# Performance work log

Measured on AMD Instinct MI355X. Metric: run time of the kernel, lower is better.

## Reference

```python
import jax, jax.numpy as jnp
import numpy as np

B, L, E, H, D = 32, 512, 256, 8, 64
SCALE = int(D ** 0.5)  # matches TF: int(hidden_dim ** 0.5) == 8


def setup_inputs() -> dict:
    key = jax.random.key(0)
    ks = jax.random.split(key, 6)
    return {
        "x": jax.random.normal(ks[0], (B, L, E), dtype=jnp.float32),
        "positional": jax.random.normal(ks[1], (L, E), dtype=jnp.float32) * 0.02,
        "Wq": jax.random.normal(ks[2], (H, E, D), dtype=jnp.float32) * 0.05,
        "Wk": jax.random.normal(ks[3], (H, E, D), dtype=jnp.float32) * 0.05,
        "Wv": jax.random.normal(ks[4], (H, E, D), dtype=jnp.float32) * 0.05,
        "Wo": jax.random.normal(ks[5], (H * D, E), dtype=jnp.float32) * 0.05,
    }


def reference(x, positional, Wq, Wk, Wv, Wo):
    act = jnp.tanh  # activation='tanh'
    xp = x + positional                                   # [B,L,E]
    # Batched per-head projections with activation applied post-matmul
    q = act(jnp.einsum('ble,hed->bhld', xp, Wq))          # [B,H,L,D]
    k = act(jnp.einsum('ble,hed->bhld', xp, Wk))
    v = act(jnp.einsum('ble,hed->bhld', xp, Wv))
    score = jnp.einsum('bhqd,bhkd->bhqk', q, k) / SCALE   # [B,H,L,L]
    attn = jax.nn.softmax(score, axis=-1)
    out = jnp.einsum('bhqk,bhkd->bhqd', attn, v)          # [B,H,L,D]
    # concat heads along last axis (head-major) -> [B,L,H*D]
    out = jnp.transpose(out, (0, 2, 1, 3)).reshape(B, L, H * D)
    return jnp.einsum('blf,fe->ble', out, Wo) + act(xp)   # [B,L,E]
```

## Files before the change

kernel.cpp:

```cpp
#include <hip/hip_runtime.h>
#include <cstdint>

#define NB 32
#define NL 512
#define NE 256
#define NH 8
#define ND 64
#define NM 16384
#define NHD 512

using half8  = __attribute__((ext_vector_type(8))) _Float16;
using half4  = __attribute__((ext_vector_type(4))) _Float16;
using f32x4  = __attribute__((ext_vector_type(4))) float;
using f32x16 = __attribute__((ext_vector_type(16))) float;

__device__ __forceinline__ f32x4 mfma16(half8 a, half8 b, f32x4 c) {
    return __builtin_amdgcn_mfma_f32_16x16x32_f16(a, b, c, 0, 0, 0);
}
__device__ __forceinline__ f32x16 mfma32(half8 a, half8 b, f32x16 c) {
    return __builtin_amdgcn_mfma_f32_32x32x16_f16(a, b, c, 0, 0, 0);
}
__device__ __forceinline__ void cp16_g2l(const void* g, void* l) {
    __builtin_amdgcn_global_load_lds(
        (const __attribute__((address_space(1))) void*)g,
        (__attribute__((address_space(3))) void*)l, 16, 0, 0);
}
__device__ __forceinline__ float fast_tanh(float x) {
    float xc = fminf(fmaxf(x, -9.f), 9.f);
    float t = __expf(2.f * xc);
    return (t - 1.f) * __builtin_amdgcn_rcpf(t + 1.f);
}

__global__ __launch_bounds__(256) void prep(
        const float* __restrict__ x, const float* __restrict__ pos,
        const float* __restrict__ Wq, const float* __restrict__ Wk,
        const float* __restrict__ Wv, const float* __restrict__ Wo,
        _Float16* __restrict__ wqkv, _Float16* __restrict__ woh,
        _Float16* __restrict__ xph) {
    int bid = blockIdx.x;
    if (bid < 2048) {
        int idx = bid * 256 + threadIdx.x;
        if (idx < 1536 * 256) {
            int n = idx >> 8, e = idx & 255;
            int s = n >> 9, h = (n >> 6) & 7, d = n & 63;
            const float* W = (s == 0) ? Wq : (s == 1) ? Wk : Wv;
            wqkv[idx] = (_Float16)W[(h * NE + e) * ND + d];
        } else {
            int j = idx - 1536 * 256;
            int e = j >> 9, f = j & 511;
            woh[j] = (_Float16)Wo[f * NE + e];
        }
    } else {
        int i = ((bid - 2048) * 256 + threadIdx.x) * 4;
        float4 xv = *(const float4*)(x + i);
        float4 pv = *(const float4*)(pos + (i & (NL * NE - 1)));
        half4 o;
        o[0] = (_Float16)(xv.x + pv.x);
        o[1] = (_Float16)(xv.y + pv.y);
        o[2] = (_Float16)(xv.z + pv.z);
        o[3] = (_Float16)(xv.w + pv.w);
        *(half4*)(xph + i) = o;
    }
}

__global__ __launch_bounds__(256) void proj_gemm(
        const _Float16* __restrict__ wqkv, const _Float16* __restrict__ xph,
        _Float16* __restrict__ q_all, _Float16* __restrict__ k_all,
        _Float16* __restrict__ vT) {
    __shared__ _Float16 Alds[128 * 64];
    __shared__ _Float16 Blds[128 * 64];
    int tid = threadIdx.x;
    int w = tid >> 6, l = tid & 63;
    int bid = blockIdx.x;
    int xcd = bid & 7, local = bid >> 3;
    int tn = local % 12;
    int tm = xcd * 16 + local / 12;
    int wn = w >> 1, wm = w & 1;
    int m16 = l & 15, g = l >> 4;
    bool isv = (tn >= 8);
    int lrow8 = l >> 3;
    int kc16 = (l & 7) ^ lrow8;
    f32x4 acc[4][4] = {};

    for (int kt = 0; kt < 4; ++kt) {
#pragma unroll
        for (int i = 0; i < 4; ++i) {
            int cA = w * 4 + i;
            int row = cA * 8 + lrow8;
            cp16_g2l(wqkv + (size_t)(tn * 128 + row) * 256 + kt * 64 + kc16 * 8,
                     Alds + cA * 512);
            cp16_g2l(xph + (size_t)(tm * 128 + row) * 256 + kt * 64 + kc16 * 8,
                     Blds + cA * 512);
        }
        __syncthreads();
#pragma unroll
        for (int ks = 0; ks < 2; ++ks) {
            half8 af[4], bf[4];
#pragma unroll
            for (int f = 0; f < 4; ++f) {
                int ra = wn * 64 + f * 16 + m16;
                int rb = wm * 64 + f * 16 + m16;
                af[f] = *(const half8*)(Alds + ra * 64 + (((ks * 4 + g) ^ (ra & 7)) << 3));
                bf[f] = *(const half8*)(Blds + rb * 64 + (((ks * 4 + g) ^ (rb & 7)) << 3));
            }
            if (!isv) {
#pragma unroll
                for (int nf = 0; nf < 4; ++nf)
#pragma unroll
                    for (int mf = 0; mf < 4; ++mf)
                        acc[nf][mf] = mfma16(af[nf], bf[mf], acc[nf][mf]);
            } else {
#pragma unroll
                for (int nf = 0; nf < 4; ++nf)
#pragma unroll
                    for (int mf = 0; mf < 4; ++mf)
                        acc[nf][mf] = mfma16(bf[mf], af[nf], acc[nf][mf]);
            }
        }
        __syncthreads();
    }
    if (!isv) {
        _Float16* dst = (tn < 4) ? q_all : k_all;
#pragma unroll
        for (int nf = 0; nf < 4; ++nf) {
            int c = (tn & 3) * 128 + wn * 64 + nf * 16 + g * 4;
#pragma unroll
            for (int mf = 0; mf < 4; ++mf) {
                int m = tm * 128 + wm * 64 + mf * 16 + m16;
                f32x4 v = acc[nf][mf];
                half4 hv;
#pragma unroll
                for (int r = 0; r < 4; ++r) hv[r] = (_Float16)fast_tanh(v[r]);
                *(half4*)(dst + (size_t)m * NHD + c) = hv;
            }
        }
    } else {
#pragma unroll
        for (int nf = 0; nf < 4; ++nf) {
            int c = (tn - 8) * 128 + wn * 64 + nf * 16 + m16;
#pragma unroll
            for (int mf = 0; mf < 4; ++mf) {
                int t0 = tm * 128 + wm * 64 + mf * 16 + g * 4;
                f32x4 v = acc[nf][mf];
                half4 hv;
#pragma unroll
                for (int r = 0; r < 4; ++r) hv[r] = (_Float16)fast_tanh(v[r]);
                *(half4*)(vT + (size_t)c * NM + t0) = hv;
            }
        }
    }
}

__global__ __launch_bounds__(256, 3) void attn_kernel(
        const _Float16* __restrict__ q_all, const _Float16* __restrict__ k_all,
        const _Float16* __restrict__ vT, _Float16* __restrict__ attn_out) {
    __shared__ _Float16 Klds[2][64 * 64];
    __shared__ _Float16 Vtlds[2][64 * 64];
    __shared__ _Float16 Plds[4][32 * 64];
    int tid = threadIdx.x;
    int w = tid >> 6, l = tid & 63;
    int l31 = l & 31, hi = l >> 5;
    int bid = blockIdx.x;
    int qt = bid & 3, h = (bid >> 2) & 7, b = bid >> 5;

    int qbase = qt * 128 + w * 32;
    half8 qf[4];
    {
        const _Float16* qp = q_all + (size_t)(b * NL + qbase + l31) * NHD + h * ND + hi * 8;
#pragma unroll
        for (int ks = 0; ks < 4; ++ks) qf[ks] = *(const half8*)(qp + ks * 16);
    }

    f32x16 acc_o[2] = {};
    float mrow = -1e30f, lrow = 0.f;

    int st_row = tid >> 2;
    int st_u0 = (tid & 3) * 2;
    const _Float16* kg = k_all + (size_t)(b * NL + st_row) * NHD + h * ND + st_u0 * 8;
    const _Float16* vg = vT + (size_t)(h * ND + st_row) * NM + b * NL + st_u0 * 8;
    int so0 = st_row * 64 + ((st_u0 ^ (st_row & 7)) << 3);
    int so1 = st_row * 64 + (((st_u0 + 1) ^ (st_row & 7)) << 3);

    uint4 kv0 = *(const uint4*)(kg);
    uint4 kv1 = *(const uint4*)(kg + 8);
    uint4 vv0 = *(const uint4*)(vg);
    uint4 vv1 = *(const uint4*)(vg + 8);
    *(uint4*)&Klds[0][so0] = kv0;   *(uint4*)&Klds[0][so1] = kv1;
    *(uint4*)&Vtlds[0][so0] = vv0;  *(uint4*)&Vtlds[0][so1] = vv1;
    __syncthreads();

    for (int kt = 0; kt < 8; ++kt) {
        int cur = kt & 1;
        if (kt < 7) {
            const _Float16* kp = kg + (size_t)(kt + 1) * 64 * NHD;
            const _Float16* vp = vg + (kt + 1) * 64;
            kv0 = *(const uint4*)(kp);      kv1 = *(const uint4*)(kp + 8);
            vv0 = *(const uint4*)(vp);      vv1 = *(const uint4*)(vp + 8);
        }
        f32x16 acc_s[2] = {};
#pragma unroll
        for (int ks = 0; ks < 4; ++ks)
#pragma unroll
            for (int kb2 = 0; kb2 < 2; ++kb2) {
                int key = kb2 * 32 + l31;
                half8 kb = *(const half8*)(&Klds[cur][key * 64 + (((ks * 2 + hi) ^ (key & 7)) << 3)]);
                acc_s[kb2] = mfma32(kb, qf[ks], acc_s[kb2]);
            }
        float mx = -1e30f;
#pragma unroll
        for (int kb2 = 0; kb2 < 2; ++kb2)
#pragma unroll
            for (int j = 0; j < 16; ++j) mx = fmaxf(mx, acc_s[kb2][j]);
        mx = fmaxf(mx, __shfl_xor(mx, 32));
        mx *= 0.125f;
        if (!__all(mx <= mrow + 8.f)) {
            float mn = fmaxf(mrow, mx);
            float alpha = __expf(mrow - mn);
            mrow = mn;
            lrow *= alpha;
            float aq[16];
#pragma unroll
            for (int c = 0; c < 4; ++c)
#pragma unroll
                for (int r = 0; r < 4; ++r)
                    aq[c * 4 + r] = __shfl(alpha, c * 8 + hi * 4 + r);
#pragma unroll
            for (int d2 = 0; d2 < 2; ++d2)
#pragma unroll
                for (int j = 0; j < 16; ++j) acc_o[d2][j] *= aq[j];
        }
        float rs = 0.f;
#pragma unroll
        for (int kb2 = 0; kb2 < 2; ++kb2)
#pragma unroll
            for (int c = 0; c < 4; ++c) {
                half4 hv;
#pragma unroll
                for (int r = 0; r < 4; ++r) {
                    float p = __expf(acc_s[kb2][c * 4 + r] * 0.125f - mrow);
                    rs += p;
                    hv[r] = (_Float16)p;
                }
                int u = kb2 * 4 + c;
                *(half4*)(&Plds[w][l31 * 64 + ((u ^ (l31 & 7)) << 3) + hi * 4]) = hv;
            }
        rs += __shfl_xor(rs, 32);
        lrow += rs;
#pragma unroll
        for (int ks = 0; ks < 4; ++ks) {
            half8 pa = *(const half8*)(&Plds[w][l31 * 64 + (((ks * 2 + hi) ^ (l31 & 7)) << 3)]);
#pragma unroll
            for (int d2 = 0; d2 < 2; ++d2) {
                int d = d2 * 32 + l31;
                half8 vb = *(const half8*)(&Vtlds[cur][d * 64 + (((ks * 2 + hi) ^ (d & 7)) << 3)]);
                acc_o[d2] = mfma32(pa, vb, acc_o[d2]);
            }
        }
        if (kt < 7) {
            int nxt = cur ^ 1;
            *(uint4*)&Klds[nxt][so0] = kv0;   *(uint4*)&Klds[nxt][so1] = kv1;
            *(uint4*)&Vtlds[nxt][so0] = vv0;  *(uint4*)&Vtlds[nxt][so1] = vv1;
            __syncthreads();
        }
    }
    size_t orow0 = (size_t)(b * NL + qbase);
#pragma unroll
    for (int c = 0; c < 4; ++c)
#pragma unroll
        for (int r = 0; r < 4; ++r) {
            int qrow = c * 8 + hi * 4 + r;
            float inv = 1.f / __shfl(lrow, qrow);
#pragma unroll
            for (int d2 = 0; d2 < 2; ++d2)
                attn_out[(orow0 + qrow) * NHD + h * ND + d2 * 32 + l31] =
                    (_Float16)(acc_o[d2][c * 4 + r] * inv);
        }
}

__global__ __launch_bounds__(256) void final_gemm(
        const _Float16* __restrict__ woh, const _Float16* __restrict__ attn,
        const float* __restrict__ x, const float* __restrict__ pos,
        float* __restrict__ out) {
    __shared__ _Float16 Alds[128 * 64];
    __shared__ _Float16 Blds[64 * 64];
    int tid = threadIdx.x;
    int w = tid >> 6, l = tid & 63;
    int tn = blockIdx.x & 1, tm = blockIdx.x >> 1;
    int wn = w >> 1, wm = w & 1;
    int m16 = l & 15, g = l >> 4;
    int lrow8 = l >> 3;
    int kc16 = (l & 7) ^ lrow8;
    f32x4 acc[4][2] = {};

    for (int kt = 0; kt < 8; ++kt) {
#pragma unroll
        for (int i = 0; i < 4; ++i) {
            int cA = w * 4 + i;
            int row = cA * 8 + lrow8;
            cp16_g2l(woh + (size_t)(tn * 128 + row) * 512 + kt * 64 + kc16 * 8,
                     Alds + cA * 512);
        }
#pragma unroll
        for (int i = 0; i < 2; ++i) {
            int cB = w * 2 + i;
            int row = cB * 8 + lrow8;
            cp16_g2l(attn + (size_t)(tm * 64 + row) * 512 + kt * 64 + kc16 * 8,
                     Blds + cB * 512);
        }
        __syncthreads();
#pragma unroll
        for (int ks = 0; ks < 2; ++ks) {
            half8 af[4], bf[2];
#pragma unroll
            for (int f = 0; f < 4; ++f) {
                int ra = wn * 64 + f * 16 + m16;
                af[f] = *(const half8*)(Alds + ra * 64 + (((ks * 4 + g) ^ (ra & 7)) << 3));
            }
#pragma unroll
            for (int f = 0; f < 2; ++f) {
                int rb = wm * 32 + f * 16 + m16;
                bf[f] = *(const half8*)(Blds + rb * 64 + (((ks * 4 + g) ^ (rb & 7)) << 3));
            }
#pragma unroll
            for (int nf = 0; nf < 4; ++nf)
#pragma unroll
                for (int mf = 0; mf < 2; ++mf)
                    acc[nf][mf] = mfma16(af[nf], bf[mf], acc[nf][mf]);
        }
        __syncthreads();
    }
#pragma unroll
    for (int nf = 0; nf < 4; ++nf) {
        int e = tn * 128 + wn * 64 + nf * 16 + g * 4;
#pragma unroll
        for (int mf = 0; mf < 2; ++mf) {
            int m = tm * 64 + wm * 32 + mf * 16 + m16;
            int lr = m & (NL - 1);
            float4 xv = *(const float4*)(x + (size_t)m * NE + e);
            float4 pv = *(const float4*)(pos + (size_t)lr * NE + e);
            f32x4 v = acc[nf][mf];
            float4 o;
            o.x = v[0] + fast_tanh(xv.x + pv.x);
            o.y = v[1] + fast_tanh(xv.y + pv.y);
            o.z = v[2] + fast_tanh(xv.z + pv.z);
            o.w = v[3] + fast_tanh(xv.w + pv.w);
            *(float4*)(out + (size_t)m * NE + e) = o;
        }
    }
}

extern "C" void kernel_launch(void* const* d_in, const int* in_sizes, int n_in,
                              void* d_out, int out_size, void* d_ws, size_t ws_size,
                              hipStream_t stream) {
    const float* x   = (const float*)d_in[0];
    const float* pos = (const float*)d_in[1];
    const float* Wq  = (const float*)d_in[2];
    const float* Wk  = (const float*)d_in[3];
    const float* Wv  = (const float*)d_in[4];
    const float* Wo  = (const float*)d_in[5];
    float* out = (float*)d_out;

    char* ws = (char*)d_ws;
    _Float16* xph   = (_Float16*)(ws);
    _Float16* wqkv  = (_Float16*)(ws + 8388608);
    _Float16* woh   = (_Float16*)(ws + 9175040);
    _Float16* q_all = (_Float16*)(ws + 9437184);
    _Float16* k_all = (_Float16*)(ws + 26214400);
    _Float16* vT    = (_Float16*)(ws + 42991616);
    _Float16* attn  = (_Float16*)(ws + 59768832);

    prep<<<dim3(6144), dim3(256), 0, stream>>>(x, pos, Wq, Wk, Wv, Wo, wqkv, woh, xph);
    proj_gemm<<<dim3(12 * 128), dim3(256), 0, stream>>>(wqkv, xph, q_all, k_all, vT);
    attn_kernel<<<dim3(1024), dim3(256), 0, stream>>>(q_all, k_all, vT, attn);
    final_gemm<<<dim3(512), dim3(256), 0, stream>>>(woh, attn, x, pos, out);
}
```

Baseline: 84.27 us.

## Double-buffer GEMM LDS tiles, raise MFMA priority, reuse fp16 xp in epilogue

```diff
diff --git a/kernel.cpp b/kernel.cpp
--- a/kernel.cpp
+++ b/kernel.cpp
@@ -67,8 +67,8 @@
         const _Float16* __restrict__ wqkv, const _Float16* __restrict__ xph,
         _Float16* __restrict__ q_all, _Float16* __restrict__ k_all,
         _Float16* __restrict__ vT) {
-    __shared__ _Float16 Alds[128 * 64];
-    __shared__ _Float16 Blds[128 * 64];
+    __shared__ _Float16 Alds[2][128 * 64];
+    __shared__ _Float16 Blds[2][128 * 64];
     int tid = threadIdx.x;
     int w = tid >> 6, l = tid & 63;
     int bid = blockIdx.x;
@@ -82,17 +82,24 @@
     int kc16 = (l & 7) ^ lrow8;
     f32x4 acc[4][4] = {};
 
+    const _Float16* Ag = wqkv + (size_t)tn * 128 * 256;
+    const _Float16* Bg = xph + (size_t)tm * 128 * 256;
+
+#define PROJ_STAGE(kt, buf)                                                   \
+    _Pragma("unroll") for (int i = 0; i < 4; ++i) {                           \
+        int cA = w * 4 + i;                                                   \
+        int row = cA * 8 + lrow8;                                             \
+        cp16_g2l(Ag + (size_t)row * 256 + (kt) * 64 + kc16 * 8,               \
+                 &Alds[buf][cA * 512]);                                       \
+        cp16_g2l(Bg + (size_t)row * 256 + (kt) * 64 + kc16 * 8,               \
+                 &Blds[buf][cA * 512]);                                       \
+    }
+
+    PROJ_STAGE(0, 0);
+    __syncthreads();
+    int cur = 0;
     for (int kt = 0; kt < 4; ++kt) {
-#pragma unroll
-        for (int i = 0; i < 4; ++i) {
-            int cA = w * 4 + i;
-            int row = cA * 8 + lrow8;
-            cp16_g2l(wqkv + (size_t)(tn * 128 + row) * 256 + kt * 64 + kc16 * 8,
-                     Alds + cA * 512);
-            cp16_g2l(xph + (size_t)(tm * 128 + row) * 256 + kt * 64 + kc16 * 8,
-                     Blds + cA * 512);
-        }
-        __syncthreads();
+        if (kt < 3) { PROJ_STAGE(kt + 1, cur ^ 1); }
 #pragma unroll
         for (int ks = 0; ks < 2; ++ks) {
             half8 af[4], bf[4];
@@ -100,8 +107,8 @@
             for (int f = 0; f < 4; ++f) {
                 int ra = wn * 64 + f * 16 + m16;
                 int rb = wm * 64 + f * 16 + m16;
-                af[f] = *(const half8*)(Alds + ra * 64 + (((ks * 4 + g) ^ (ra & 7)) << 3));
-                bf[f] = *(const half8*)(Blds + rb * 64 + (((ks * 4 + g) ^ (rb & 7)) << 3));
+                af[f] = *(const half8*)(&Alds[cur][ra * 64 + (((ks * 4 + g) ^ (ra & 7)) << 3)]);
+                bf[f] = *(const half8*)(&Blds[cur][rb * 64 + (((ks * 4 + g) ^ (rb & 7)) << 3)]);
             }
             if (!isv) {
 #pragma unroll
@@ -118,7 +125,9 @@
             }
         }
         __syncthreads();
-    }
+        cur ^= 1;
+    }
+#undef PROJ_STAGE
     if (!isv) {
         _Float16* dst = (tn < 4) ? q_all : k_all;
 #pragma unroll
@@ -198,6 +207,7 @@
             vv0 = *(const uint4*)(vp);      vv1 = *(const uint4*)(vp + 8);
         }
         f32x16 acc_s[2] = {};
+        __builtin_amdgcn_s_setprio(1);
 #pragma unroll
         for (int ks = 0; ks < 4; ++ks)
 #pragma unroll
@@ -206,6 +216,7 @@
                 half8 kb = *(const half8*)(&Klds[cur][key * 64 + (((ks * 2 + hi) ^ (key & 7)) << 3)]);
                 acc_s[kb2] = mfma32(kb, qf[ks], acc_s[kb2]);
             }
+        __builtin_amdgcn_s_setprio(0);
         float mx = -1e30f;
 #pragma unroll
         for (int kb2 = 0; kb2 < 2; ++kb2)
@@ -246,6 +257,7 @@
             }
         rs += __shfl_xor(rs, 32);
         lrow += rs;
+        __builtin_amdgcn_s_setprio(1);
 #pragma unroll
         for (int ks = 0; ks < 4; ++ks) {
             half8 pa = *(const half8*)(&Plds[w][l31 * 64 + (((ks * 2 + hi) ^ (l31 & 7)) << 3)]);
@@ -256,6 +268,7 @@
                 acc_o[d2] = mfma32(pa, vb, acc_o[d2]);
             }
         }
+        __builtin_amdgcn_s_setprio(0);
         if (kt < 7) {
             int nxt = cur ^ 1;
             *(uint4*)&Klds[nxt][so0] = kv0;   *(uint4*)&Klds[nxt][so1] = kv1;
@@ -279,10 +292,9 @@
 
 __global__ __launch_bounds__(256) void final_gemm(
         const _Float16* __restrict__ woh, const _Float16* __restrict__ attn,
-        const float* __restrict__ x, const float* __restrict__ pos,
-        float* __restrict__ out) {
-    __shared__ _Float16 Alds[128 * 64];
-    __shared__ _Float16 Blds[64 * 64];
+        const _Float16* __restrict__ xph, float* __restrict__ out) {
+    __shared__ _Float16 Alds[2][128 * 64];
+    __shared__ _Float16 Blds[2][64 * 64];
     int tid = threadIdx.x;
     int w = tid >> 6, l = tid & 63;
     int tn = blockIdx.x & 1, tm = blockIdx.x >> 1;
@@ -292,34 +304,40 @@
     int kc16 = (l & 7) ^ lrow8;
     f32x4 acc[4][2] = {};
 
+    const _Float16* Ag = woh + (size_t)tn * 128 * 512;
+    const _Float16* Bg = attn + (size_t)tm * 64 * 512;
+
+#define FIN_STAGE(kt, buf)                                                    \
+    _Pragma("unroll") for (int i = 0; i < 4; ++i) {                           \
+        int cA = w * 4 + i;                                                   \
+        int row = cA * 8 + lrow8;                                             \
+        cp16_g2l(Ag + (size_t)row * 512 + (kt) * 64 + kc16 * 8,               \
+                 &Alds[buf][cA * 512]);                                       \
+    }                                                                         \
+    _Pragma("unroll") for (int i = 0; i < 2; ++i) {                           \
+        int cB = w * 2 + i;                                                   \
+        int row = cB * 8 + lrow8;                                             \
+        cp16_g2l(Bg + (size_t)row * 512 + (kt) * 64 + kc16 * 8,               \
+                 &Blds[buf][cB * 512]);                                       \
+    }
+
+    FIN_STAGE(0, 0);
+    __syncthreads();
+    int cur = 0;
     for (int kt = 0; kt < 8; ++kt) {
-#pragma unroll
-        for (int i = 0; i < 4; ++i) {
-            int cA = w * 4 + i;
-            int row = cA * 8 + lrow8;
-            cp16_g2l(woh + (size_t)(tn * 128 + row) * 512 + kt * 64 + kc16 * 8,
-                     Alds + cA * 512);
-        }
-#pragma unroll
-        for (int i = 0; i < 2; ++i) {
-            int cB = w * 2 + i;
-            int row = cB * 8 + lrow8;
-            cp16_g2l(attn + (size_t)(tm * 64 + row) * 512 + kt * 64 + kc16 * 8,
-                     Blds + cB * 512);
-        }
-        __syncthreads();
+        if (kt < 7) { FIN_STAGE(kt + 1, cur ^ 1); }
 #pragma unroll
         for (int ks = 0; ks < 2; ++ks) {
             half8 af[4], bf[2];
 #pragma unroll
             for (int f = 0; f < 4; ++f) {
                 int ra = wn * 64 + f * 16 + m16;
-                af[f] = *(const half8*)(Alds + ra * 64 + (((ks * 4 + g) ^ (ra & 7)) << 3));
+                af[f] = *(const half8*)(&Alds[cur][ra * 64 + (((ks * 4 + g) ^ (ra & 7)) << 3)]);
             }
 #pragma unroll
             for (int f = 0; f < 2; ++f) {
                 int rb = wm * 32 + f * 16 + m16;
-                bf[f] = *(const half8*)(Blds + rb * 64 + (((ks * 4 + g) ^ (rb & 7)) << 3));
+                bf[f] = *(const half8*)(&Blds[cur][rb * 64 + (((ks * 4 + g) ^ (rb & 7)) << 3)]);
             }
 #pragma unroll
             for (int nf = 0; nf < 4; ++nf)
@@ -328,22 +346,22 @@
                     acc[nf][mf] = mfma16(af[nf], bf[mf], acc[nf][mf]);
         }
         __syncthreads();
-    }
+        cur ^= 1;
+    }
+#undef FIN_STAGE
 #pragma unroll
     for (int nf = 0; nf < 4; ++nf) {
         int e = tn * 128 + wn * 64 + nf * 16 + g * 4;
 #pragma unroll
         for (int mf = 0; mf < 2; ++mf) {
             int m = tm * 64 + wm * 32 + mf * 16 + m16;
-            int lr = m & (NL - 1);
-            float4 xv = *(const float4*)(x + (size_t)m * NE + e);
-            float4 pv = *(const float4*)(pos + (size_t)lr * NE + e);
+            half4 hx = *(const half4*)(xph + (size_t)m * NE + e);
             f32x4 v = acc[nf][mf];
             float4 o;
-            o.x = v[0] + fast_tanh(xv.x + pv.x);
-            o.y = v[1] + fast_tanh(xv.y + pv.y);
-            o.z = v[2] + fast_tanh(xv.z + pv.z);
-            o.w = v[3] + fast_tanh(xv.w + pv.w);
+            o.x = v[0] + fast_tanh((float)hx[0]);
+            o.y = v[1] + fast_tanh((float)hx[1]);
+            o.z = v[2] + fast_tanh((float)hx[2]);
+            o.w = v[3] + fast_tanh((float)hx[3]);
             *(float4*)(out + (size_t)m * NE + e) = o;
         }
     }
@@ -372,5 +390,5 @@
     prep<<<dim3(6144), dim3(256), 0, stream>>>(x, pos, Wq, Wk, Wv, Wo, wqkv, woh, xph);
     proj_gemm<<<dim3(12 * 128), dim3(256), 0, stream>>>(wqkv, xph, q_all, k_all, vT);
     attn_kernel<<<dim3(1024), dim3(256), 0, stream>>>(q_all, k_all, vT, attn);
-    final_gemm<<<dim3(512), dim3(256), 0, stream>>>(woh, attn, x, pos, out);
-}
+    final_gemm<<<dim3(512), dim3(256), 0, stream>>>(woh, attn, xph, out);
+}
```

Result: slower. 86.85 us (+3.1%).
